# Kernel optimization log

Measured on AMD Instinct MI355X. Metric: run time of the kernel, lower is better.

Reference implementation:

```python
import jax, jax.numpy as jnp
import numpy as np


def setup_inputs() -> dict:
    key = jax.random.key(0)
    ks = jax.random.split(key, 6)
    B, T, H, U = 32, 2048, 1024, 1024
    return {
        "query": jax.random.normal(ks[0], (1, B, H), dtype=jnp.float32),
        "values": jax.random.normal(ks[1], (B, T, H), dtype=jnp.float32),
        "W_w": jax.random.normal(ks[2], (U, 2 * H), dtype=jnp.float32) * (1.0 / np.sqrt(2 * H)),
        "W_b": jax.random.normal(ks[3], (U,), dtype=jnp.float32) * 0.02,
        "V_w": jax.random.normal(ks[4], (1, U), dtype=jnp.float32) * (1.0 / np.sqrt(U)),
        "V_b": jax.random.normal(ks[5], (1,), dtype=jnp.float32) * 0.02,
    }


def reference(query, values, W_w, W_b, V_w, V_b):
    # query: [1, B, H] -> [B, H]; values: [B, T, H]
    q = query[0]  # squeeze dim 0
    H = values.shape[-1]
    # Split W over the concat dim instead of materializing cat([values, q_rep]):
    # cat @ W.T == values @ W[:, :H].T + q @ W[:, H:].T  (same math as torch)
    Wv, Wq = W_w[:, :H], W_w[:, H:]
    pre = (jnp.einsum("bth,uh->btu", values, Wv)
           + jnp.einsum("bh,uh->bu", q, Wq)[:, None, :]
           + W_b)  # [B, T, U]
    score = jnp.tanh(pre) @ V_w[0] + V_b[0]  # [B, T]
    attention_weights = jax.nn.softmax(score, axis=1)[..., None]  # [B, T, 1]
    context_vector = jnp.sum(attention_weights * values, axis=1)  # [B, H]
    return (context_vector, attention_weights)
```

## Files before the change

kernel.cpp:

```cpp
#include <hip/hip_runtime.h>
#include <hip/hip_bf16.h>


#define B_DIM 32
#define T_DIM 2048
#define H_DIM 1024
#define U_DIM 1024

typedef __bf16 bf16x8 __attribute__((ext_vector_type(8)));
typedef float f32x4 __attribute__((ext_vector_type(4)));

__device__ __forceinline__ unsigned int f2bf(float f) {
    unsigned int u = __float_as_uint(f);
    return (u + 0x7FFFu + ((u >> 16) & 1u)) >> 16;
}

__device__ __forceinline__ unsigned int cvt2(float lo, float hi) {
    unsigned int r;
    asm volatile("v_cvt_pk_bf16_f32 %0, %1, %2" : "=v"(r) : "v"(lo), "v"(hi));
    return r;
}

__device__ __forceinline__ float fast_tanh(float x) {
    x = fminf(9.f, fmaxf(-9.f, x));
    float e = __expf(2.f * x);
    return 1.f - 2.f * __frcp_rn(e + 1.f);
}

__device__ __forceinline__ void glds16(const void* g, void* l) {
    __builtin_amdgcn_global_load_lds(
        (const __attribute__((address_space(1))) unsigned int*)g,
        (__attribute__((address_space(3))) unsigned int*)l, 16, 0, 0);
}

__global__ void prep_wv_kernel(const float* __restrict__ W_w,
                               unsigned short* __restrict__ wv) {
    int u = blockIdx.x;
    int tid = threadIdx.x;
    float4 x = reinterpret_cast<const float4*>(W_w + (size_t)u * 2 * H_DIM)[tid];
    uint2 p;
    p.x = f2bf(x.x) | (f2bf(x.y) << 16);
    p.y = f2bf(x.z) | (f2bf(x.w) << 16);
    reinterpret_cast<uint2*>(wv)[(size_t)u * (H_DIM / 4) + tid] = p;
}

__global__ void prep_c_kernel(const float* __restrict__ q,
                              const float* __restrict__ W_w,
                              const float* __restrict__ W_b,
                              float* __restrict__ cvec,
                              float* __restrict__ ctx) {
    __shared__ float4 q_sh[4][H_DIM / 4];
    int bg = blockIdx.y;
    int u0 = blockIdx.x * 64;
    int tid = threadIdx.x;
    int lane = tid & 63, w = tid >> 6;
    ctx[(size_t)(blockIdx.y * 16 + blockIdx.x) * 256 + tid] = 0.f;
#pragma unroll
    for (int i = 0; i < 4; i++)
        q_sh[i][tid] = reinterpret_cast<const float4*>(
            q + (size_t)(bg * 4 + i) * H_DIM)[tid];
    __syncthreads();
#pragma unroll
    for (int i = 0; i < 16; i++) {
        int u = u0 + w * 16 + i;
        const float4* wr = reinterpret_cast<const float4*>(W_w + (size_t)u * 2 * H_DIM + H_DIM);
        float s0 = 0.f, s1 = 0.f, s2 = 0.f, s3 = 0.f;
#pragma unroll
        for (int j = 0; j < 4; j++) {
            float4 wv4 = wr[j * 64 + lane];
            float4 qa = q_sh[0][j * 64 + lane];
            float4 qb = q_sh[1][j * 64 + lane];
            float4 qc = q_sh[2][j * 64 + lane];
            float4 qd = q_sh[3][j * 64 + lane];
            s0 += wv4.x * qa.x + wv4.y * qa.y + wv4.z * qa.z + wv4.w * qa.w;
            s1 += wv4.x * qb.x + wv4.y * qb.y + wv4.z * qb.z + wv4.w * qb.w;
            s2 += wv4.x * qc.x + wv4.y * qc.y + wv4.z * qc.z + wv4.w * qc.w;
            s3 += wv4.x * qd.x + wv4.y * qd.y + wv4.z * qd.z + wv4.w * qd.w;
        }
#pragma unroll
        for (int off = 32; off >= 1; off >>= 1) {
            s0 += __shfl_xor(s0, off, 64);
            s1 += __shfl_xor(s1, off, 64);
            s2 += __shfl_xor(s2, off, 64);
            s3 += __shfl_xor(s3, off, 64);
        }
        if (lane == 0) {
            float bb = W_b[u];
            cvec[(size_t)(bg * 4 + 0) * U_DIM + u] = s0 + bb;
            cvec[(size_t)(bg * 4 + 1) * U_DIM + u] = s1 + bb;
            cvec[(size_t)(bg * 4 + 2) * U_DIM + u] = s2 + bb;
            cvec[(size_t)(bg * 4 + 3) * U_DIM + u] = s3 + bb;
        }
    }
}

__global__ __launch_bounds__(512, 2)
void gemm_score_kernel(const float* __restrict__ values,
                       const unsigned short* __restrict__ wv,
                       const float* __restrict__ cvec,
                       const float* __restrict__ Vw,
                       float* __restrict__ score_part) {
    __shared__ __align__(16) unsigned short a_sh[4][256 * 32];
    __shared__ __align__(16) unsigned short b_sh[4][256 * 32];

    const int tid = threadIdx.x;
    const int lane = tid & 63;
    const int w = tid >> 6;
    const int col = lane & 15;
    const int quad = lane >> 4;
    const int wr = w >> 2;
    const int wc = w & 3;

    const int work = (blockIdx.x & 7) * 128 + (blockIdx.x >> 3);
    const int mtile = work >> 2;
    const int ntile = work & 3;
    const int m0 = mtile * 256;
    const int b = m0 >> 11;

    f32x4 acc[8][4];
    const f32x4 zero4 = {0.f, 0.f, 0.f, 0.f};
#pragma unroll
    for (int mt = 0; mt < 8; mt++)
#pragma unroll
        for (int nt = 0; nt < 4; nt++) acc[mt][nt] = zero4;

    const int arow = tid >> 1;
    const int akh = tid & 1;
    const float4* agl = reinterpret_cast<const float4*>(values) +
                        ((size_t)(m0 + arow) * 256 + akh * 4);
    const int as0 = (akh * 2) ^ (arow & 3);

    const int bn0 = ntile * 256 + w * 32 + (lane >> 2);
    const int bslot = ((lane & 3) ^ ((lane >> 2) & 3)) * 16;
    const char* bsrc0 = (const char*)wv + (size_t)bn0 * 2048 + bslot;
    const char* bsrc1 = bsrc0 + 16 * 2048;

    const int fro = (quad ^ (col & 3)) * 8;
    const int aro = (wr * 128 + col) * 32 + fro;
    const int bro = (wc * 64 + col) * 32 + fro;

#define AISSUE(SET, TS) do {                                                   \
        SET[0] = agl[(TS) * 8 + 0]; SET[1] = agl[(TS) * 8 + 1];                \
        SET[2] = agl[(TS) * 8 + 2]; SET[3] = agl[(TS) * 8 + 3];                \
    } while (0)

#define BISSUE(TS) do {                                                        \
        glds16(bsrc0 + (size_t)(TS) * 64, &b_sh[(TS) & 3][w * 1024]);          \
        glds16(bsrc1 + (size_t)(TS) * 64, &b_sh[(TS) & 3][w * 1024 + 512]);    \
    } while (0)

#define AWRITE(SET, TS) do {                                                   \
        uint4 p0, p1;                                                          \
        p0.x = cvt2(SET[0].x, SET[0].y); p0.y = cvt2(SET[0].z, SET[0].w);      \
        p0.z = cvt2(SET[1].x, SET[1].y); p0.w = cvt2(SET[1].z, SET[1].w);      \
        p1.x = cvt2(SET[2].x, SET[2].y); p1.y = cvt2(SET[2].z, SET[2].w);      \
        p1.z = cvt2(SET[3].x, SET[3].y); p1.w = cvt2(SET[3].z, SET[3].w);      \
        *reinterpret_cast<uint4*>(&a_sh[(TS) & 3][arow * 32 + as0 * 8]) = p0;  \
        *reinterpret_cast<uint4*>(&a_sh[(TS) & 3][arow * 32 + (as0 ^ 1) * 8]) = p1; \
    } while (0)

#define KSTEP_CORE(T) do {                                                     \
        const int cb_ = (T) & 3;                                               \
        bf16x8 af[8], bf[4];                                                   \
        _Pragma("unroll")                                                      \
        for (int mt = 0; mt < 8; mt++)                                         \
            af[mt] = *reinterpret_cast<const bf16x8*>(&a_sh[cb_][aro + mt * 512]); \
        _Pragma("unroll")                                                      \
        for (int nt = 0; nt < 4; nt++)                                         \
            bf[nt] = *reinterpret_cast<const bf16x8*>(&b_sh[cb_][bro + nt * 512]); \
        __builtin_amdgcn_s_setprio(1);                                         \
        _Pragma("unroll")                                                      \
        for (int nt = 0; nt < 4; nt++)                                         \
            _Pragma("unroll")                                                  \
            for (int mt = 0; mt < 8; mt++)                                     \
                acc[mt][nt] = __builtin_amdgcn_mfma_f32_16x16x32_bf16(         \
                    af[mt], bf[nt], acc[mt][nt], 0, 0, 0);                     \
        __builtin_amdgcn_s_setprio(0);                                         \
    } while (0)

    float4 sA[4], sB[4];

    AISSUE(sA, 0); BISSUE(0);
    AISSUE(sB, 1); BISSUE(1);
    AWRITE(sA, 0);

    for (int tt = 0; tt < 30; tt += 2) {
        AISSUE(sA, tt + 2); BISSUE(tt + 2);
        asm volatile("s_waitcnt vmcnt(6)" ::: "memory");
        AWRITE(sB, tt + 1);
        asm volatile("s_waitcnt lgkmcnt(0)" ::: "memory");
        __builtin_amdgcn_s_barrier();
        asm volatile("" ::: "memory");
        KSTEP_CORE(tt);
        AISSUE(sB, tt + 3); BISSUE(tt + 3);
        asm volatile("s_waitcnt vmcnt(6)" ::: "memory");
        AWRITE(sA, tt + 2);
        asm volatile("s_waitcnt lgkmcnt(0)" ::: "memory");
        __builtin_amdgcn_s_barrier();
        asm volatile("" ::: "memory");
        KSTEP_CORE(tt + 1);
    }
    AWRITE(sB, 31);
    asm volatile("s_waitcnt lgkmcnt(0)" ::: "memory");
    __builtin_amdgcn_s_barrier();
    asm volatile("" ::: "memory");
    KSTEP_CORE(30);
    asm volatile("s_waitcnt vmcnt(0)" ::: "memory");
    __builtin_amdgcn_s_barrier();
    asm volatile("" ::: "memory");
    KSTEP_CORE(31);

    __syncthreads();

#undef AISSUE
#undef BISSUE
#undef AWRITE
#undef KSTEP_CORE

    float* sc = reinterpret_cast<float*>(a_sh);
    float cv[4], vwv[4];
#pragma unroll
    for (int nt = 0; nt < 4; nt++) {
        int n = ntile * 256 + wc * 64 + nt * 16 + col;
        cv[nt] = cvec[(size_t)b * U_DIM + n];
        vwv[nt] = Vw[n];
    }
#pragma unroll
    for (int mt = 0; mt < 8; mt++) {
#pragma unroll
        for (int j = 0; j < 4; j++) {
            float s = 0.f;
#pragma unroll
            for (int nt = 0; nt < 4; nt++)
                s += fast_tanh(acc[mt][nt][j] + cv[nt]) * vwv[nt];
            s += __shfl_xor(s, 1, 64);
            s += __shfl_xor(s, 2, 64);
            s += __shfl_xor(s, 4, 64);
            s += __shfl_xor(s, 8, 64);
            if (col == 0) sc[(wr * 128 + mt * 16 + quad * 4 + j) * 4 + wc] = s;
        }
    }
    __syncthreads();
    if (tid < 256) {
        float s = sc[tid * 4] + sc[tid * 4 + 1] + sc[tid * 4 + 2] + sc[tid * 4 + 3];
        score_part[(size_t)ntile * (B_DIM * T_DIM) + m0 + tid] = s;
    }
}

__global__ void ctx_sm_kernel(const float* __restrict__ values,
                              const float* __restrict__ score_part,
                              float* __restrict__ aw,
                              float* __restrict__ ctx) {
    int tc = blockIdx.x;
    int b = blockIdx.y;
    int tid = threadIdx.x;
    int lane = tid & 63, w = tid >> 6;
    __shared__ float redm[4];
    __shared__ float reds[4];
    __shared__ float aw_sh[128];
    const float* sp = score_part + (size_t)b * T_DIM;
    float loc[8];
    float m = -1e30f;
#pragma unroll
    for (int i = 0; i < 8; i++) {
        int t = tid + i * 256;
        float s = sp[t] + sp[65536 + t] + sp[131072 + t] + sp[196608 + t];
        loc[i] = s;
        m = fmaxf(m, s);
    }
#pragma unroll
    for (int off = 32; off >= 1; off >>= 1) m = fmaxf(m, __shfl_xor(m, off, 64));
    if (lane == 0) redm[w] = m;
    __syncthreads();
    m = fmaxf(fmaxf(redm[0], redm[1]), fmaxf(redm[2], redm[3]));
    float sum = 0.f;
#pragma unroll
    for (int i = 0; i < 8; i++) {
        loc[i] = __expf(loc[i] - m);
        sum += loc[i];
    }
#pragma unroll
    for (int off = 32; off >= 1; off >>= 1) sum += __shfl_xor(sum, off, 64);
    if (lane == 0) reds[w] = sum;
    __syncthreads();
    sum = reds[0] + reds[1] + reds[2] + reds[3];
    float inv = 1.0f / sum;
    if (tid < 128) {
        int t = tc * 128 + tid;
        float s = sp[t] + sp[65536 + t] + sp[131072 + t] + sp[196608 + t];
        float av = __expf(s - m) * inv;
        aw[(size_t)b * T_DIM + t] = av;
        aw_sh[tid] = av;
    }
    __syncthreads();
    const float4* v4 = reinterpret_cast<const float4*>(
                           values + ((size_t)b * T_DIM + tc * 128) * H_DIM) + tid;
    float4 a = make_float4(0.f, 0.f, 0.f, 0.f);
#pragma unroll 4
    for (int t = 0; t < 128; t++) {
        float wgt = aw_sh[t];
        float4 vv = v4[(size_t)t * (H_DIM / 4)];
        a.x += wgt * vv.x; a.y += wgt * vv.y;
        a.z += wgt * vv.z; a.w += wgt * vv.w;
    }
    float* cp = ctx + (size_t)b * H_DIM + tid * 4;
    atomicAdd(cp + 0, a.x);
    atomicAdd(cp + 1, a.y);
    atomicAdd(cp + 2, a.z);
    atomicAdd(cp + 3, a.w);
}

extern "C" void kernel_launch(void* const* d_in, const int* in_sizes, int n_in,
                              void* d_out, int out_size, void* d_ws, size_t ws_size,
                              hipStream_t stream) {
    const float* query  = (const float*)d_in[0];
    const float* values = (const float*)d_in[1];
    const float* W_w    = (const float*)d_in[2];
    const float* W_b    = (const float*)d_in[3];
    const float* V_w    = (const float*)d_in[4];

    float* out = (float*)d_out;
    char* ws = (char*)d_ws;
    float* cvec            = (float*)(ws);
    unsigned short* wv     = (unsigned short*)(ws + 131072);
    float* score_part      = (float*)(ws + 131072 + 2097152);
    float* ctx = out;
    float* aw  = out + B_DIM * H_DIM;

    prep_wv_kernel<<<U_DIM, 256, 0, stream>>>(W_w, wv);
    prep_c_kernel<<<dim3(U_DIM / 64, B_DIM / 4), 256, 0, stream>>>(query, W_w, W_b, cvec, ctx);
    gemm_score_kernel<<<1024, 512, 0, stream>>>(values, wv, cvec, V_w, score_part);
    ctx_sm_kernel<<<dim3(16, B_DIM), 256, 0, stream>>>(values, score_part, aw, ctx);
}
```

Before: 594.3 us.

## Stream fp32 values directly into LDS and convert to bf16 at fragment load

The GEMM kernel now loads the fp32 A tile straight into LDS with global_load_lds, matching the B tile, instead of staging it through registers with a bf16 conversion and ds_write. Conversion to bf16 moves to the point where fragments are read from LDS. The pipeline becomes a 3-stage ring with new XOR swizzles. The aim is to free VGPRs and cut the register-staged write path, at the cost of twice the LDS traffic and space for A and redundant conversions repeated across waves. Separately, the context kernel splits T into 64-row chunks across twice as many blocks to raise parallelism, which doubles the atomics.

```diff
diff --git a/kernel.cpp b/kernel.cpp
--- a/kernel.cpp
+++ b/kernel.cpp
@@ -27,7 +27,7 @@
     return 1.f - 2.f * __frcp_rn(e + 1.f);
 }
 
-__device__ __forceinline__ void glds16(const void* g, void* l) {
+__device__ __forceinline__ void glds16(const void* g, const void* l) {
     __builtin_amdgcn_global_load_lds(
         (const __attribute__((address_space(1))) unsigned int*)g,
         (__attribute__((address_space(3))) unsigned int*)l, 16, 0, 0);
@@ -100,8 +100,8 @@
                        const float* __restrict__ cvec,
                        const float* __restrict__ Vw,
                        float* __restrict__ score_part) {
-    __shared__ __align__(16) unsigned short a_sh[4][256 * 32];
-    __shared__ __align__(16) unsigned short b_sh[4][256 * 32];
+    __shared__ __align__(16) float a_sh[3][256 * 32];
+    __shared__ __align__(16) unsigned short b_sh[3][128 * 64];
 
     const int tid = threadIdx.x;
     const int lane = tid & 63;
@@ -124,50 +124,48 @@
 #pragma unroll
         for (int nt = 0; nt < 4; nt++) acc[mt][nt] = zero4;
 
-    const int arow = tid >> 1;
-    const int akh = tid & 1;
-    const float4* agl = reinterpret_cast<const float4*>(values) +
-                        ((size_t)(m0 + arow) * 256 + akh * 4);
-    const int as0 = (akh * 2) ^ (arow & 3);
-
-    const int bn0 = ntile * 256 + w * 32 + (lane >> 2);
-    const int bslot = ((lane & 3) ^ ((lane >> 2) & 3)) * 16;
-    const char* bsrc0 = (const char*)wv + (size_t)bn0 * 2048 + bslot;
-    const char* bsrc1 = bsrc0 + 16 * 2048;
-
-    const int fro = (quad ^ (col & 3)) * 8;
-    const int aro = (wr * 128 + col) * 32 + fro;
-    const int bro = (wc * 64 + col) * 32 + fro;
-
-#define AISSUE(SET, TS) do {                                                   \
-        SET[0] = agl[(TS) * 8 + 0]; SET[1] = agl[(TS) * 8 + 1];                \
-        SET[2] = agl[(TS) * 8 + 2]; SET[3] = agl[(TS) * 8 + 3];                \
+    const int l8 = lane >> 3, l7 = lane & 7;
+    const int xa = l7 ^ l8;
+    const char* asrc = (const char*)values +
+        (size_t)(m0 + w * 32 + l8) * 4096 + xa * 16;
+    const char* bsrc = (const char*)wv +
+        (size_t)((size_t)ntile * 256 + w * 32 + 2 * l8 + (xa >> 2)) * 2048 +
+        (xa & 3) * 16;
+
+    const int aoff = (wr * 128 + col) * 128 + (((quad * 2) ^ (col & 7)) * 16);
+    const int boff = (wc * 32 + (col >> 1)) * 128 +
+                     (((((col & 1) << 2) | quad) ^ (col >> 1)) * 16);
+
+#define STAGE(SBUF, KS) do {                                                   \
+        glds16(asrc + (size_t)(KS) * 128,          &a_sh[SBUF][(w * 32) * 32]);      \
+        glds16(asrc + (size_t)(KS) * 128 + 32768,  &a_sh[SBUF][(w * 32 + 8) * 32]);  \
+        glds16(asrc + (size_t)(KS) * 128 + 65536,  &a_sh[SBUF][(w * 32 + 16) * 32]); \
+        glds16(asrc + (size_t)(KS) * 128 + 98304,  &a_sh[SBUF][(w * 32 + 24) * 32]); \
+        glds16(bsrc + (size_t)(KS) * 64,           &b_sh[SBUF][(w * 16) * 64]);      \
+        glds16(bsrc + (size_t)(KS) * 64 + 32768,   &b_sh[SBUF][(w * 16 + 8) * 64]);  \
     } while (0)
 
-#define BISSUE(TS) do {                                                        \
-        glds16(bsrc0 + (size_t)(TS) * 64, &b_sh[(TS) & 3][w * 1024]);          \
-        glds16(bsrc1 + (size_t)(TS) * 64, &b_sh[(TS) & 3][w * 1024 + 512]);    \
-    } while (0)
-
-#define AWRITE(SET, TS) do {                                                   \
-        uint4 p0, p1;                                                          \
-        p0.x = cvt2(SET[0].x, SET[0].y); p0.y = cvt2(SET[0].z, SET[0].w);      \
-        p0.z = cvt2(SET[1].x, SET[1].y); p0.w = cvt2(SET[1].z, SET[1].w);      \
-        p1.x = cvt2(SET[2].x, SET[2].y); p1.y = cvt2(SET[2].z, SET[2].w);      \
-        p1.z = cvt2(SET[3].x, SET[3].y); p1.w = cvt2(SET[3].z, SET[3].w);      \
-        *reinterpret_cast<uint4*>(&a_sh[(TS) & 3][arow * 32 + as0 * 8]) = p0;  \
-        *reinterpret_cast<uint4*>(&a_sh[(TS) & 3][arow * 32 + (as0 ^ 1) * 8]) = p1; \
-    } while (0)
-
-#define KSTEP_CORE(T) do {                                                     \
-        const int cb_ = (T) & 3;                                               \
+#define KSTEP(BUF, VM, STG, SBUF, KS) do {                                     \
+        asm volatile("s_waitcnt vmcnt(" #VM ")" ::: "memory");                 \
+        __builtin_amdgcn_s_barrier();                                          \
+        asm volatile("" ::: "memory");                                         \
+        if (STG) STAGE(SBUF, KS);                                              \
         bf16x8 af[8], bf[4];                                                   \
+        const char* ab_ = (const char*)&a_sh[BUF][0];                          \
+        const char* bb_ = (const char*)&b_sh[BUF][0];                          \
         _Pragma("unroll")                                                      \
-        for (int mt = 0; mt < 8; mt++)                                         \
-            af[mt] = *reinterpret_cast<const bf16x8*>(&a_sh[cb_][aro + mt * 512]); \
+        for (int mt = 0; mt < 8; mt++) {                                       \
+            int o0 = aoff + mt * 2048;                                         \
+            float4 f0 = *reinterpret_cast<const float4*>(ab_ + o0);            \
+            float4 f1 = *reinterpret_cast<const float4*>(ab_ + (o0 ^ 16));     \
+            uint4 u_;                                                          \
+            u_.x = cvt2(f0.x, f0.y); u_.y = cvt2(f0.z, f0.w);                  \
+            u_.z = cvt2(f1.x, f1.y); u_.w = cvt2(f1.z, f1.w);                  \
+            af[mt] = __builtin_bit_cast(bf16x8, u_);                           \
+        }                                                                      \
         _Pragma("unroll")                                                      \
         for (int nt = 0; nt < 4; nt++)                                         \
-            bf[nt] = *reinterpret_cast<const bf16x8*>(&b_sh[cb_][bro + nt * 512]); \
+            bf[nt] = *reinterpret_cast<const bf16x8*>(bb_ + boff + nt * 1024); \
         __builtin_amdgcn_s_setprio(1);                                         \
         _Pragma("unroll")                                                      \
         for (int nt = 0; nt < 4; nt++)                                         \
@@ -178,44 +176,21 @@
         __builtin_amdgcn_s_setprio(0);                                         \
     } while (0)
 
-    float4 sA[4], sB[4];
-
-    AISSUE(sA, 0); BISSUE(0);
-    AISSUE(sB, 1); BISSUE(1);
-    AWRITE(sA, 0);
-
-    for (int tt = 0; tt < 30; tt += 2) {
-        AISSUE(sA, tt + 2); BISSUE(tt + 2);
-        asm volatile("s_waitcnt vmcnt(6)" ::: "memory");
-        AWRITE(sB, tt + 1);
-        asm volatile("s_waitcnt lgkmcnt(0)" ::: "memory");
-        __builtin_amdgcn_s_barrier();
-        asm volatile("" ::: "memory");
-        KSTEP_CORE(tt);
-        AISSUE(sB, tt + 3); BISSUE(tt + 3);
-        asm volatile("s_waitcnt vmcnt(6)" ::: "memory");
-        AWRITE(sA, tt + 2);
-        asm volatile("s_waitcnt lgkmcnt(0)" ::: "memory");
-        __builtin_amdgcn_s_barrier();
-        asm volatile("" ::: "memory");
-        KSTEP_CORE(tt + 1);
-    }
-    AWRITE(sB, 31);
-    asm volatile("s_waitcnt lgkmcnt(0)" ::: "memory");
-    __builtin_amdgcn_s_barrier();
-    asm volatile("" ::: "memory");
-    KSTEP_CORE(30);
-    asm volatile("s_waitcnt vmcnt(0)" ::: "memory");
-    __builtin_amdgcn_s_barrier();
-    asm volatile("" ::: "memory");
-    KSTEP_CORE(31);
-
-    __syncthreads();
-
-#undef AISSUE
-#undef BISSUE
-#undef AWRITE
-#undef KSTEP_CORE
+    STAGE(0, 0);
+    STAGE(1, 1);
+
+    for (int t3 = 0; t3 < 30; t3 += 3) {
+        KSTEP(0, 6, 1, 2, t3 + 2);
+        KSTEP(1, 6, 1, 0, t3 + 3);
+        KSTEP(2, 6, 1, 1, t3 + 4);
+    }
+    KSTEP(0, 6, 0, 0, 0);
+    KSTEP(1, 0, 0, 0, 0);
+
+    __syncthreads();
+
+#undef STAGE
+#undef KSTEP
 
     float* sc = reinterpret_cast<float*>(a_sh);
     float cv[4], vwv[4];
@@ -257,7 +232,7 @@
     int lane = tid & 63, w = tid >> 6;
     __shared__ float redm[4];
     __shared__ float reds[4];
-    __shared__ float aw_sh[128];
+    __shared__ float aw_sh[64];
     const float* sp = score_part + (size_t)b * T_DIM;
     float loc[8];
     float m = -1e30f;
@@ -285,8 +260,8 @@
     __syncthreads();
     sum = reds[0] + reds[1] + reds[2] + reds[3];
     float inv = 1.0f / sum;
-    if (tid < 128) {
-        int t = tc * 128 + tid;
+    if (tid < 64) {
+        int t = tc * 64 + tid;
         float s = sp[t] + sp[65536 + t] + sp[131072 + t] + sp[196608 + t];
         float av = __expf(s - m) * inv;
         aw[(size_t)b * T_DIM + t] = av;
@@ -294,10 +269,10 @@
     }
     __syncthreads();
     const float4* v4 = reinterpret_cast<const float4*>(
-                           values + ((size_t)b * T_DIM + tc * 128) * H_DIM) + tid;
+                           values + ((size_t)b * T_DIM + tc * 64) * H_DIM) + tid;
     float4 a = make_float4(0.f, 0.f, 0.f, 0.f);
 #pragma unroll 4
-    for (int t = 0; t < 128; t++) {
+    for (int t = 0; t < 64; t++) {
         float wgt = aw_sh[t];
         float4 vv = v4[(size_t)t * (H_DIM / 4)];
         a.x += wgt * vv.x; a.y += wgt * vv.y;
@@ -330,5 +305,5 @@
     prep_wv_kernel<<<U_DIM, 256, 0, stream>>>(W_w, wv);
     prep_c_kernel<<<dim3(U_DIM / 64, B_DIM / 4), 256, 0, stream>>>(query, W_w, W_b, cvec, ctx);
     gemm_score_kernel<<<1024, 512, 0, stream>>>(values, wv, cvec, V_w, score_part);
-    ctx_sm_kernel<<<dim3(16, B_DIM), 256, 0, stream>>>(values, score_part, aw, ctx);
-}
+    ctx_sm_kernel<<<dim3(32, B_DIM), 256, 0, stream>>>(values, score_part, aw, ctx);
+}
```

Result: slower. 645.5 us (+8.6%).
